# Performance work log

Hardware: AMD Instinct MI355X
Metric: run time of the kernel (lower is better)

The kernel has to match this reference:

```python
import jax, jax.numpy as jnp
import numpy as np

N_VAR, N_CONS, E = 50000, 50000, 800000
F, FE, H, ITERS = 64, 8, 128, 2  # node feat, edge feat, hidden, gnn iterations


def _mlp(x, w1, b1, w2, b2):
    # MultilayerPerceptron([in, hidden, out]) = Linear -> ReLU -> Linear
    return jax.nn.relu(x @ w1 + b1) @ w2 + b2


def setup_inputs() -> dict:
    key = jax.random.key(0)
    ks = jax.random.split(key, 17)

    def w(k, shape, fan_in):
        return jax.random.normal(k, shape, jnp.float32) / np.sqrt(fan_in).astype(np.float32)

    msg_in = 2 * F + FE   # 136
    upd_in = 2 * F        # 128
    return {
        "var_feat": jax.random.normal(ks[0], (N_VAR, F), jnp.float32),
        "cons_feat": jax.random.normal(ks[1], (N_CONS, F), jnp.float32),
        "edge_feat": jax.random.normal(ks[2], (E, FE), jnp.float32),
        "edge_var": jax.random.randint(ks[3], (E,), 0, N_VAR),
        "edge_cons": jax.random.randint(ks[4], (E,), 0, N_CONS),
        # messenger MLP (note: original code uses var messenger for BOTH sides)
        "w_msg1": w(ks[5], (ITERS, msg_in, H), msg_in),
        "b_msg1": jnp.zeros((ITERS, H), jnp.float32),
        "w_msg2": w(ks[6], (ITERS, H, F), H),
        "b_msg2": jnp.zeros((ITERS, F), jnp.float32),
        # var update MLP
        "w_vupd1": w(ks[7], (ITERS, upd_in, H), upd_in),
        "b_vupd1": jnp.zeros((ITERS, H), jnp.float32),
        "w_vupd2": w(ks[8], (ITERS, H, F), H),
        "b_vupd2": jnp.zeros((ITERS, F), jnp.float32),
        # cons update MLP
        "w_cupd1": w(ks[9], (ITERS, upd_in, H), upd_in),
        "b_cupd1": jnp.zeros((ITERS, H), jnp.float32),
        "w_cupd2": w(ks[10], (ITERS, H, F), H),
        "b_cupd2": jnp.zeros((ITERS, F), jnp.float32),
    }


def reference(var_feat, cons_feat, edge_feat, edge_var, edge_cons,
              w_msg1, b_msg1, w_msg2, b_msg2,
              w_vupd1, b_vupd1, w_vupd2, b_vupd2,
              w_cupd1, b_cupd1, w_cupd2, b_cupd2):
    for i in range(ITERS):
        vs = var_feat[edge_var]    # [E, F] gather of var endpoint feats
        cs = cons_feat[edge_cons]  # [E, F] gather of cons endpoint feats
        # --- var-node message pass: (var_feat, neighbor cons_feat, edge_feat) ---
        m_v = _mlp(jnp.concatenate([vs, cs, edge_feat], axis=1),
                   w_msg1[i], b_msg1[i], w_msg2[i], b_msg2[i])        # [E, F]
        agg_v = jax.ops.segment_sum(m_v, edge_var, num_segments=N_VAR)  # zeros for isolated nodes
        new_var = _mlp(jnp.concatenate([var_feat, agg_v], axis=1),
                       w_vupd1[i], b_vupd1[i], w_vupd2[i], b_vupd2[i])
        # --- cons-node message pass (uses var messenger weights, as in source) ---
        m_c = _mlp(jnp.concatenate([cs, vs, edge_feat], axis=1),
                   w_msg1[i], b_msg1[i], w_msg2[i], b_msg2[i])        # [E, F]
        agg_c = jax.ops.segment_sum(m_c, edge_cons, num_segments=N_CONS)
        new_cons = _mlp(jnp.concatenate([cons_feat, agg_c], axis=1),
                        w_cupd1[i], b_cupd1[i], w_cupd2[i], b_cupd2[i])
        var_feat, cons_feat = new_var, new_cons
    return var_feat, cons_feat
```

## Files before the change

### kernel.cpp

```cpp
#include <hip/hip_runtime.h>

#define N_NODES 50000
#define E_EDGES 800000
#define F 64
#define FE 8
#define H 128
#define MSG_IN 136
#define XPAD 168
#define HPW 68
#define NXP 136

typedef short bf16x8 __attribute__((ext_vector_type(8)));
typedef float f32x4 __attribute__((ext_vector_type(4)));

__device__ __forceinline__ ushort f2bf(float f) {
  uint u = __float_as_uint(f);
  u = (u + 0x7FFFu + ((u >> 16) & 1u)) >> 16;
  return (ushort)u;
}
__device__ __forceinline__ uint pack2(float lo, float hi) {
  uint r;
  asm("v_cvt_pk_bf16_f32 %0, %1, %2" : "=v"(r) : "v"(lo), "v"(hi));
  return r;
}
__device__ __forceinline__ void atomic_pk_add_bf16(ushort* addr, uint data) {
  asm volatile("global_atomic_pk_add_bf16 %0, %1, off" :: "v"(addr), "v"(data) : "memory");
}

__global__ __launch_bounds__(256)
void cvt_feats(const float* __restrict__ a, const float* __restrict__ b,
               ushort* __restrict__ oa, ushort* __restrict__ ob) {
  const int n4 = N_NODES * F / 4;
  for (int i = blockIdx.x * blockDim.x + threadIdx.x; i < n4; i += gridDim.x * blockDim.x) {
    const float4 va = ((const float4*)a)[i];
    const float4 vb = ((const float4*)b)[i];
    ((uint2*)oa)[i] = make_uint2(pack2(va.x, va.y), pack2(va.z, va.w));
    ((uint2*)ob)[i] = make_uint2(pack2(vb.x, vb.y), pack2(vb.z, vb.w));
  }
}

__global__ __launch_bounds__(256, 3)
void edge_pass_mfma(const ushort* __restrict__ vfeat, const ushort* __restrict__ cfeat,
                    const float* __restrict__ efeat,
                    const int* __restrict__ ev, const int* __restrict__ ec,
                    const float* __restrict__ w1, const float* __restrict__ b1,
                    const float* __restrict__ w2, const float* __restrict__ b2,
                    ushort* __restrict__ aggv, ushort* __restrict__ aggc)
{
  __shared__ __align__(16) ushort sX[64 * XPAD];
  __shared__ __align__(16) uint  sH[64 * HPW];
  __shared__ int sIv[64], sIc[64];

  const int t = threadIdx.x;
  const int wid = t >> 6, l15 = t & 15, hi = (t >> 4) & 3;
  const int eh = wid >> 1, fh = wid & 1;

  bf16x8 bf1[2][5];
  #pragma unroll
  for (int n = 0; n < 2; ++n) {
    const int col = wid * 32 + n * 16 + l15;
    #pragma unroll
    for (int kb = 0; kb < 5; ++kb)
      #pragma unroll
      for (int i = 0; i < 8; ++i) {
        const int kg = kb * 32 + hi * 8 + i;
        float val = 0.f;
        if (kg < MSG_IN) val = w1[kg * H + col];
        else if (kg == MSG_IN) val = b1[col];
        bf1[n][kb][i] = (short)f2bf(val);
      }
  }
  bf16x8 bf2[2][4];
  #pragma unroll
  for (int fbl = 0; fbl < 2; ++fbl) {
    const int col = fh * 32 + 2 * l15 + fbl;
    #pragma unroll
    for (int kb = 0; kb < 4; ++kb)
      #pragma unroll
      for (int i = 0; i < 8; ++i) {
        const int p = hi * 8 + i;
        const int kl = (p >> 1) | ((p & 1) << 4);
        bf2[fbl][kb][i] = (short)f2bf(w2[(kb * 32 + kl) * F + col]);
      }
  }
  const float bb2[2] = { b2[fh * 32 + 2 * l15], b2[fh * 32 + 2 * l15 + 1] };

  {
    uint* xu = (uint*)sX;
    for (int i = t; i < 64 * 16; i += 256) {
      const int row = i >> 4, u = i & 15;
      xu[row * (XPAD / 2) + 68 + u] = (u == 0) ? 0x00003F80u : 0u;
    }
  }

  const int r = t >> 2, q = t & 3;
  const int g = gridDim.x;
  const int nTiles = E_EDGES / 64;
  int tile = blockIdx.x;
  int ivC = ev[tile * 64 + r], icC = ec[tile * 64 + r];

  constexpr int perm[5] = {2, 3, 0, 1, 4};

  for (; tile < nTiles; tile += g) {
    {
      const uint4* vp = (const uint4*)(vfeat + (size_t)ivC * F);
      const uint4* cp = (const uint4*)(cfeat + (size_t)icC * F);
      uint4* xr4 = (uint4*)((uint*)sX + r * (XPAD / 2));
      xr4[q * 2]     = vp[q * 2];
      xr4[q * 2 + 1] = vp[q * 2 + 1];
      xr4[8 + q * 2]     = cp[q * 2];
      xr4[8 + q * 2 + 1] = cp[q * 2 + 1];
      if (q == 0) {
        const float4* ep = (const float4*)(efeat + (size_t)(tile * 64 + r) * FE);
        const float4 e0 = ep[0], e1 = ep[1];
        xr4[16] = make_uint4(pack2(e0.x, e0.y), pack2(e0.z, e0.w),
                             pack2(e1.x, e1.y), pack2(e1.z, e1.w));
      }
    }
    const int nt2 = (tile + g < nTiles) ? tile + g : tile;
    const int ivN = ev[nt2 * 64 + r];
    const int icN = ec[nt2 * 64 + r];
    __syncthreads();
    if (q == 0) { sIv[r] = ivC; sIc[r] = icC; }

    f32x4 acc[4][2];
    const ushort* sHu = (const ushort*)sH;

    #pragma unroll
    for (int m = 0; m < 4; ++m)
      #pragma unroll
      for (int n = 0; n < 2; ++n) acc[m][n] = (f32x4)(0.f);
    #pragma unroll
    for (int kb = 0; kb < 5; ++kb)
      #pragma unroll
      for (int m = 0; m < 4; ++m) {
        const bf16x8 a = *(const bf16x8*)&sX[(m * 16 + l15) * XPAD + kb * 32 + hi * 8];
        #pragma unroll
        for (int n = 0; n < 2; ++n)
          acc[m][n] = __builtin_amdgcn_mfma_f32_16x16x32_bf16(a, bf1[n][kb], acc[m][n], 0, 0, 0);
      }
    #pragma unroll
    for (int m = 0; m < 4; ++m)
      #pragma unroll
      for (int rr = 0; rr < 4; ++rr) {
        const int e = m * 16 + hi * 4 + rr;
        sH[e * HPW + wid * 16 + l15] =
            pack2(fmaxf(acc[m][0][rr], 0.f), fmaxf(acc[m][1][rr], 0.f));
      }
    __syncthreads();

    {
      f32x4 a2[2][2];
      #pragma unroll
      for (int mm = 0; mm < 2; ++mm) { a2[mm][0] = (f32x4)(0.f); a2[mm][1] = (f32x4)(0.f); }
      #pragma unroll
      for (int kb = 0; kb < 4; ++kb)
        #pragma unroll
        for (int mm = 0; mm < 2; ++mm) {
          const int e = (eh * 2 + mm) * 16 + l15;
          const bf16x8 a = *(const bf16x8*)&sHu[e * (HPW * 2) + kb * 32 + hi * 8];
          a2[mm][0] = __builtin_amdgcn_mfma_f32_16x16x32_bf16(a, bf2[0][kb], a2[mm][0], 0, 0, 0);
          a2[mm][1] = __builtin_amdgcn_mfma_f32_16x16x32_bf16(a, bf2[1][kb], a2[mm][1], 0, 0, 0);
        }
      #pragma unroll
      for (int mm = 0; mm < 2; ++mm)
        #pragma unroll
        for (int rr = 0; rr < 4; ++rr) {
          const int idx = sIv[(eh * 2 + mm) * 16 + hi * 4 + rr];
          ushort* dst = aggv + (size_t)idx * F + fh * 32 + 2 * l15;
          atomic_pk_add_bf16(dst, pack2(a2[mm][0][rr] + bb2[0], a2[mm][1][rr] + bb2[1]));
        }
    }

    #pragma unroll
    for (int m = 0; m < 4; ++m)
      #pragma unroll
      for (int n = 0; n < 2; ++n) acc[m][n] = (f32x4)(0.f);
    #pragma unroll
    for (int kb = 0; kb < 5; ++kb)
      #pragma unroll
      for (int m = 0; m < 4; ++m) {
        const bf16x8 a = *(const bf16x8*)&sX[(m * 16 + l15) * XPAD + kb * 32 + hi * 8];
        #pragma unroll
        for (int n = 0; n < 2; ++n)
          acc[m][n] = __builtin_amdgcn_mfma_f32_16x16x32_bf16(a, bf1[n][perm[kb]], acc[m][n], 0, 0, 0);
      }
    __syncthreads();
    #pragma unroll
    for (int m = 0; m < 4; ++m)
      #pragma unroll
      for (int rr = 0; rr < 4; ++rr) {
        const int e = m * 16 + hi * 4 + rr;
        sH[e * HPW + wid * 16 + l15] =
            pack2(fmaxf(acc[m][0][rr], 0.f), fmaxf(acc[m][1][rr], 0.f));
      }
    __syncthreads();

    {
      f32x4 a2[2][2];
      #pragma unroll
      for (int mm = 0; mm < 2; ++mm) { a2[mm][0] = (f32x4)(0.f); a2[mm][1] = (f32x4)(0.f); }
      #pragma unroll
      for (int kb = 0; kb < 4; ++kb)
        #pragma unroll
        for (int mm = 0; mm < 2; ++mm) {
          const int e = (eh * 2 + mm) * 16 + l15;
          const bf16x8 a = *(const bf16x8*)&sHu[e * (HPW * 2) + kb * 32 + hi * 8];
          a2[mm][0] = __builtin_amdgcn_mfma_f32_16x16x32_bf16(a, bf2[0][kb], a2[mm][0], 0, 0, 0);
          a2[mm][1] = __builtin_amdgcn_mfma_f32_16x16x32_bf16(a, bf2[1][kb], a2[mm][1], 0, 0, 0);
        }
      #pragma unroll
      for (int mm = 0; mm < 2; ++mm)
        #pragma unroll
        for (int rr = 0; rr < 4; ++rr) {
          const int idx = sIc[(eh * 2 + mm) * 16 + hi * 4 + rr];
          ushort* dst = aggc + (size_t)idx * F + fh * 32 + 2 * l15;
          atomic_pk_add_bf16(dst, pack2(a2[mm][0][rr] + bb2[0], a2[mm][1][rr] + bb2[1]));
        }
    }
    ivC = ivN; icC = icN;
  }
}

__global__ __launch_bounds__(256, 2)
void node_update_dual(ushort* __restrict__ vfeat, const ushort* __restrict__ vagg,
                      ushort* __restrict__ cfeat, const ushort* __restrict__ cagg,
                      const float* __restrict__ w1v, const float* __restrict__ b1v,
                      const float* __restrict__ w2v, const float* __restrict__ b2v,
                      const float* __restrict__ w1c, const float* __restrict__ b1c,
                      const float* __restrict__ w2c, const float* __restrict__ b2c,
                      float* __restrict__ outv, float* __restrict__ outc,
                      int writeF32)
{
  __shared__ __align__(16) ushort sX[64 * NXP];
  __shared__ __align__(16) uint  sH[64 * HPW];

  const int half = (N_NODES + 63) / 64;
  const bool isC = (int)blockIdx.x >= half;
  const int tile = isC ? blockIdx.x - half : blockIdx.x;
  ushort* feat = isC ? cfeat : vfeat;
  const ushort* agg = isC ? cagg : vagg;
  const float* w1 = isC ? w1c : w1v;  const float* b1 = isC ? b1c : b1v;
  const float* w2 = isC ? w2c : w2v;  const float* b2 = isC ? b2c : b2v;
  float* outf = isC ? outc : outv;

  const int t = threadIdx.x;
  const int wid = t >> 6, l15 = t & 15, hi = (t >> 4) & 3;

  bf16x8 bf1[2][4];
  #pragma unroll
  for (int n = 0; n < 2; ++n) {
    const int col = wid * 32 + n * 16 + l15;
    #pragma unroll
    for (int kb = 0; kb < 4; ++kb)
      #pragma unroll
      for (int i = 0; i < 8; ++i)
        bf1[n][kb][i] = (short)f2bf(w1[(kb * 32 + hi * 8 + i) * H + col]);
  }
  bf16x8 bf2[2][2][4];
  #pragma unroll
  for (int gg = 0; gg < 2; ++gg)
    #pragma unroll
    for (int fbl = 0; fbl < 2; ++fbl) {
      const int col = gg * 32 + 2 * l15 + fbl;
      #pragma unroll
      for (int kb = 0; kb < 4; ++kb)
        #pragma unroll
        for (int i = 0; i < 8; ++i) {
          const int p = hi * 8 + i;
          const int kl = (p >> 1) | ((p & 1) << 4);
          bf2[gg][fbl][kb][i] = (short)f2bf(w2[(kb * 32 + kl) * F + col]);
        }
    }
  const float bb1[2] = { b1[wid * 32 + l15], b1[wid * 32 + 16 + l15] };
  float bb2[2][2];
  #pragma unroll
  for (int gg = 0; gg < 2; ++gg) {
    bb2[gg][0] = b2[gg * 32 + 2 * l15];
    bb2[gg][1] = b2[gg * 32 + 2 * l15 + 1];
  }

  const int r = t >> 2, q = t & 3;
  {
    const int node = tile * 64 + r;
    const int nc = node < N_NODES ? node : N_NODES - 1;
    const uint4* fp = (const uint4*)(feat + (size_t)nc * F);
    const uint4* ap = (const uint4*)(agg + (size_t)nc * F);
    uint4* xr4 = (uint4*)&sX[r * NXP];
    xr4[q * 2]     = fp[q * 2];
    xr4[q * 2 + 1] = fp[q * 2 + 1];
    xr4[8 + q * 2]     = ap[q * 2];
    xr4[8 + q * 2 + 1] = ap[q * 2 + 1];
  }
  __syncthreads();

  f32x4 aV[4][2];
  #pragma unroll
  for (int m = 0; m < 4; ++m)
    #pragma unroll
    for (int n = 0; n < 2; ++n) aV[m][n] = (f32x4)(0.f);
  #pragma unroll
  for (int kb = 0; kb < 4; ++kb)
    #pragma unroll
    for (int m = 0; m < 4; ++m) {
      const bf16x8 a = *(const bf16x8*)&sX[(m * 16 + l15) * NXP + kb * 32 + hi * 8];
      #pragma unroll
      for (int n = 0; n < 2; ++n)
        aV[m][n] = __builtin_amdgcn_mfma_f32_16x16x32_bf16(a, bf1[n][kb], aV[m][n], 0, 0, 0);
    }
  #pragma unroll
  for (int m = 0; m < 4; ++m)
    #pragma unroll
    for (int rr = 0; rr < 4; ++rr) {
      const int e = m * 16 + hi * 4 + rr;
      sH[e * HPW + wid * 16 + l15] =
          pack2(fmaxf(aV[m][0][rr] + bb1[0], 0.f), fmaxf(aV[m][1][rr] + bb1[1], 0.f));
    }
  __syncthreads();

  f32x4 a2[2][2];
  #pragma unroll
  for (int gg = 0; gg < 2; ++gg)
    #pragma unroll
    for (int fbl = 0; fbl < 2; ++fbl) a2[gg][fbl] = (f32x4)(0.f);
  const ushort* sHu = (const ushort*)sH;
  #pragma unroll
  for (int kb = 0; kb < 4; ++kb) {
    const int e = wid * 16 + l15;
    const bf16x8 a = *(const bf16x8*)&sHu[e * (HPW * 2) + kb * 32 + hi * 8];
    #pragma unroll
    for (int gg = 0; gg < 2; ++gg)
      #pragma unroll
      for (int fbl = 0; fbl < 2; ++fbl)
        a2[gg][fbl] = __builtin_amdgcn_mfma_f32_16x16x32_bf16(a, bf2[gg][fbl][kb], a2[gg][fbl], 0, 0, 0);
  }
  #pragma unroll
  for (int rr = 0; rr < 4; ++rr) {
    const int node = tile * 64 + wid * 16 + hi * 4 + rr;
    if (node < N_NODES) {
      #pragma unroll
      for (int gg = 0; gg < 2; ++gg) {
        const float o0 = a2[gg][0][rr] + bb2[gg][0];
        const float o1 = a2[gg][1][rr] + bb2[gg][1];
        *(uint*)&feat[(size_t)node * F + gg * 32 + 2 * l15] = pack2(o0, o1);
        if (writeF32) {
          float2 o = make_float2(o0, o1);
          *(float2*)&outf[(size_t)node * F + gg * 32 + 2 * l15] = o;
        }
      }
    }
  }
}

extern "C" void kernel_launch(void* const* d_in, const int* in_sizes, int n_in,
                              void* d_out, int out_size, void* d_ws, size_t ws_size,
                              hipStream_t stream) {
  const float* var_feat  = (const float*)d_in[0];
  const float* cons_feat = (const float*)d_in[1];
  const float* edge_feat = (const float*)d_in[2];
  const int*   ev        = (const int*)d_in[3];
  const int*   ec        = (const int*)d_in[4];
  const float* w_msg1  = (const float*)d_in[5];
  const float* b_msg1  = (const float*)d_in[6];
  const float* w_msg2  = (const float*)d_in[7];
  const float* b_msg2  = (const float*)d_in[8];
  const float* w_vupd1 = (const float*)d_in[9];
  const float* b_vupd1 = (const float*)d_in[10];
  const float* w_vupd2 = (const float*)d_in[11];
  const float* b_vupd2 = (const float*)d_in[12];
  const float* w_cupd1 = (const float*)d_in[13];
  const float* b_cupd1 = (const float*)d_in[14];
  const float* w_cupd2 = (const float*)d_in[15];
  const float* b_cupd2 = (const float*)d_in[16];

  const size_t NF = (size_t)N_NODES * F;
  ushort* aggv = (ushort*)d_ws;
  ushort* aggc = aggv + NF;
  ushort* vb   = aggc + NF;
  ushort* cb   = vb + NF;
  float* outv = (float*)d_out;
  float* outc = outv + NF;

  cvt_feats<<<512, 256, 0, stream>>>(var_feat, cons_feat, vb, cb);

  for (int it = 0; it < 2; ++it) {
    hipMemsetAsync(aggv, 0, 2 * NF * sizeof(ushort), stream);

    edge_pass_mfma<<<1024, 256, 0, stream>>>(vb, cb, edge_feat, ev, ec,
        w_msg1 + (size_t)it * MSG_IN * H, b_msg1 + (size_t)it * H,
        w_msg2 + (size_t)it * H * F,      b_msg2 + (size_t)it * F,
        aggv, aggc);

    node_update_dual<<<1564, 256, 0, stream>>>(vb, aggv, cb, aggc,
        w_vupd1 + (size_t)it * H * H, b_vupd1 + (size_t)it * H,
        w_vupd2 + (size_t)it * H * F, b_vupd2 + (size_t)it * F,
        w_cupd1 + (size_t)it * H * H, b_cupd1 + (size_t)it * H,
        w_cupd2 + (size_t)it * H * F, b_cupd2 + (size_t)it * F,
        outv, outc, it == 1 ? 1 : 0);
  }
}
```

Measured before the change: 488.9 us.

## Prefetch next tile's gathered features into registers and merge the two layer-2 phases

The gather of the next tile's var/cons/edge features is software-pipelined: they load into registers during the current tile's compute and are written to LDS at the start of the next iteration, with indices prefetched two tiles ahead. The hidden buffer is doubled so both sides' layer-1 outputs coexist, which removes two barriers and lets both layer-2 GEMMs and their atomics run in one loop. Occupancy drops from 3 to 2 blocks per SIMD and the grid is halved to 512, trading parallelism for latency hiding and more registers and LDS. A leftover dead block computes unused pointers.

```diff
diff --git a/kernel.cpp b/kernel.cpp
--- a/kernel.cpp
+++ b/kernel.cpp
@@ -39,7 +39,7 @@
   }
 }
 
-__global__ __launch_bounds__(256, 3)
+__global__ __launch_bounds__(256, 2)
 void edge_pass_mfma(const ushort* __restrict__ vfeat, const ushort* __restrict__ cfeat,
                     const float* __restrict__ efeat,
                     const int* __restrict__ ev, const int* __restrict__ ec,
@@ -48,7 +48,7 @@
                     ushort* __restrict__ aggv, ushort* __restrict__ aggc)
 {
   __shared__ __align__(16) ushort sX[64 * XPAD];
-  __shared__ __align__(16) uint  sH[64 * HPW];
+  __shared__ __align__(16) uint  sH[128 * HPW];
   __shared__ int sIv[64], sIc[64];
 
   const int t = threadIdx.x;
@@ -97,34 +97,63 @@
   const int g = gridDim.x;
   const int nTiles = E_EDGES / 64;
   int tile = blockIdx.x;
+
+  constexpr int perm[5] = {2, 3, 0, 1, 4};
+
   int ivC = ev[tile * 64 + r], icC = ec[tile * 64 + r];
-
-  constexpr int perm[5] = {2, 3, 0, 1, 4};
+  {
+    const int nt = (tile + g < nTiles) ? tile + g : tile;
+    const uint4* vp = (const uint4*)(vfeat + (size_t)ivC * F);
+    const uint4* cp = (const uint4*)(cfeat + (size_t)icC * F);
+  }
+  uint4 sv0, sv1, sc0, sc1;
+  float4 fe0, fe1;
+  {
+    const uint4* vp = (const uint4*)(vfeat + (size_t)ivC * F);
+    const uint4* cp = (const uint4*)(cfeat + (size_t)icC * F);
+    sv0 = vp[q * 2]; sv1 = vp[q * 2 + 1];
+    sc0 = cp[q * 2]; sc1 = cp[q * 2 + 1];
+    if (q == 0) {
+      const float4* ep = (const float4*)(efeat + (size_t)(tile * 64 + r) * FE);
+      fe0 = ep[0]; fe1 = ep[1];
+    }
+  }
+  int ivN, icN;
+  {
+    const int nt = (tile + g < nTiles) ? tile + g : tile;
+    ivN = ev[nt * 64 + r]; icN = ec[nt * 64 + r];
+  }
 
   for (; tile < nTiles; tile += g) {
     {
+      uint4* xr4 = (uint4*)((uint*)sX + r * (XPAD / 2));
+      xr4[q * 2]     = sv0;
+      xr4[q * 2 + 1] = sv1;
+      xr4[8 + q * 2]     = sc0;
+      xr4[8 + q * 2 + 1] = sc1;
+      if (q == 0)
+        xr4[16] = make_uint4(pack2(fe0.x, fe0.y), pack2(fe0.z, fe0.w),
+                             pack2(fe1.x, fe1.y), pack2(fe1.z, fe1.w));
+    }
+    __syncthreads();
+    if (q == 0) { sIv[r] = ivC; sIc[r] = icC; }
+
+    ivC = ivN; icC = icN;
+    {
+      const int t2 = (tile + 2 * g < nTiles) ? tile + 2 * g : tile;
+      ivN = ev[t2 * 64 + r]; icN = ec[t2 * 64 + r];
       const uint4* vp = (const uint4*)(vfeat + (size_t)ivC * F);
       const uint4* cp = (const uint4*)(cfeat + (size_t)icC * F);
-      uint4* xr4 = (uint4*)((uint*)sX + r * (XPAD / 2));
-      xr4[q * 2]     = vp[q * 2];
-      xr4[q * 2 + 1] = vp[q * 2 + 1];
-      xr4[8 + q * 2]     = cp[q * 2];
-      xr4[8 + q * 2 + 1] = cp[q * 2 + 1];
+      sv0 = vp[q * 2]; sv1 = vp[q * 2 + 1];
+      sc0 = cp[q * 2]; sc1 = cp[q * 2 + 1];
       if (q == 0) {
-        const float4* ep = (const float4*)(efeat + (size_t)(tile * 64 + r) * FE);
-        const float4 e0 = ep[0], e1 = ep[1];
-        xr4[16] = make_uint4(pack2(e0.x, e0.y), pack2(e0.z, e0.w),
-                             pack2(e1.x, e1.y), pack2(e1.z, e1.w));
-      }
-    }
-    const int nt2 = (tile + g < nTiles) ? tile + g : tile;
-    const int ivN = ev[nt2 * 64 + r];
-    const int icN = ec[nt2 * 64 + r];
-    __syncthreads();
-    if (q == 0) { sIv[r] = ivC; sIc[r] = icC; }
+        const int en = ((tile + g < nTiles) ? tile + g : tile) * 64 + r;
+        const float4* ep = (const float4*)(efeat + (size_t)en * FE);
+        fe0 = ep[0]; fe1 = ep[1];
+      }
+    }
 
     f32x4 acc[4][2];
-    const ushort* sHu = (const ushort*)sH;
 
     #pragma unroll
     for (int m = 0; m < 4; ++m)
@@ -147,30 +176,6 @@
         sH[e * HPW + wid * 16 + l15] =
             pack2(fmaxf(acc[m][0][rr], 0.f), fmaxf(acc[m][1][rr], 0.f));
       }
-    __syncthreads();
-
-    {
-      f32x4 a2[2][2];
-      #pragma unroll
-      for (int mm = 0; mm < 2; ++mm) { a2[mm][0] = (f32x4)(0.f); a2[mm][1] = (f32x4)(0.f); }
-      #pragma unroll
-      for (int kb = 0; kb < 4; ++kb)
-        #pragma unroll
-        for (int mm = 0; mm < 2; ++mm) {
-          const int e = (eh * 2 + mm) * 16 + l15;
-          const bf16x8 a = *(const bf16x8*)&sHu[e * (HPW * 2) + kb * 32 + hi * 8];
-          a2[mm][0] = __builtin_amdgcn_mfma_f32_16x16x32_bf16(a, bf2[0][kb], a2[mm][0], 0, 0, 0);
-          a2[mm][1] = __builtin_amdgcn_mfma_f32_16x16x32_bf16(a, bf2[1][kb], a2[mm][1], 0, 0, 0);
-        }
-      #pragma unroll
-      for (int mm = 0; mm < 2; ++mm)
-        #pragma unroll
-        for (int rr = 0; rr < 4; ++rr) {
-          const int idx = sIv[(eh * 2 + mm) * 16 + hi * 4 + rr];
-          ushort* dst = aggv + (size_t)idx * F + fh * 32 + 2 * l15;
-          atomic_pk_add_bf16(dst, pack2(a2[mm][0][rr] + bb2[0], a2[mm][1][rr] + bb2[1]));
-        }
-    }
 
     #pragma unroll
     for (int m = 0; m < 4; ++m)
@@ -185,18 +190,19 @@
         for (int n = 0; n < 2; ++n)
           acc[m][n] = __builtin_amdgcn_mfma_f32_16x16x32_bf16(a, bf1[n][perm[kb]], acc[m][n], 0, 0, 0);
       }
-    __syncthreads();
     #pragma unroll
     for (int m = 0; m < 4; ++m)
       #pragma unroll
       for (int rr = 0; rr < 4; ++rr) {
         const int e = m * 16 + hi * 4 + rr;
-        sH[e * HPW + wid * 16 + l15] =
+        sH[(64 + e) * HPW + wid * 16 + l15] =
             pack2(fmaxf(acc[m][0][rr], 0.f), fmaxf(acc[m][1][rr], 0.f));
       }
     __syncthreads();
 
-    {
+    const ushort* sHu = (const ushort*)sH;
+    #pragma unroll
+    for (int side = 0; side < 2; ++side) {
       f32x4 a2[2][2];
       #pragma unroll
       for (int mm = 0; mm < 2; ++mm) { a2[mm][0] = (f32x4)(0.f); a2[mm][1] = (f32x4)(0.f); }
@@ -204,21 +210,22 @@
       for (int kb = 0; kb < 4; ++kb)
         #pragma unroll
         for (int mm = 0; mm < 2; ++mm) {
-          const int e = (eh * 2 + mm) * 16 + l15;
+          const int e = side * 64 + (eh * 2 + mm) * 16 + l15;
           const bf16x8 a = *(const bf16x8*)&sHu[e * (HPW * 2) + kb * 32 + hi * 8];
           a2[mm][0] = __builtin_amdgcn_mfma_f32_16x16x32_bf16(a, bf2[0][kb], a2[mm][0], 0, 0, 0);
           a2[mm][1] = __builtin_amdgcn_mfma_f32_16x16x32_bf16(a, bf2[1][kb], a2[mm][1], 0, 0, 0);
         }
+      ushort* agg = side ? aggc : aggv;
+      const int* sI = side ? sIc : sIv;
       #pragma unroll
       for (int mm = 0; mm < 2; ++mm)
         #pragma unroll
         for (int rr = 0; rr < 4; ++rr) {
-          const int idx = sIc[(eh * 2 + mm) * 16 + hi * 4 + rr];
-          ushort* dst = aggc + (size_t)idx * F + fh * 32 + 2 * l15;
+          const int idx = sI[(eh * 2 + mm) * 16 + hi * 4 + rr];
+          ushort* dst = agg + (size_t)idx * F + fh * 32 + 2 * l15;
           atomic_pk_add_bf16(dst, pack2(a2[mm][0][rr] + bb2[0], a2[mm][1][rr] + bb2[1]));
         }
     }
-    ivC = ivN; icC = icN;
   }
 }
 
@@ -386,7 +393,7 @@
   for (int it = 0; it < 2; ++it) {
     hipMemsetAsync(aggv, 0, 2 * NF * sizeof(ushort), stream);
 
-    edge_pass_mfma<<<1024, 256, 0, stream>>>(vb, cb, edge_feat, ev, ec,
+    edge_pass_mfma<<<512, 256, 0, stream>>>(vb, cb, edge_feat, ev, ec,
         w_msg1 + (size_t)it * MSG_IN * H, b_msg1 + (size_t)it * H,
         w_msg2 + (size_t)it * H * F,      b_msg2 + (size_t)it * F,
         aggv, aggc);
```

After: 421.4 us. -13.8%, faster.
